# Kernel optimization log

Hardware: AMD Instinct MI355X
Metric: run time of the kernel (lower is better)

Reference implementation:

```python
import jax, jax.numpy as jnp
import numpy as np

N_NODES = 8192
N_EDGES = 262144
IN_DIM = 256
HID = 256
OUT_DIM = 64
PATH_DIM = 64
N_HEADS = 4


def setup_inputs() -> dict:
    key = jax.random.key(0)
    ks = jax.random.split(key, 16)
    s = 0.05
    x = jax.random.normal(ks[0], (N_NODES, IN_DIM), dtype=jnp.float32)
    edge_index = jax.random.randint(ks[1], (2, N_EDGES), 0, N_NODES, dtype=jnp.int32)
    return {
        "x": x,
        "edge_index": edge_index,
        # pathway encoder Linear(IN_DIM, PATH_DIM)
        "pe_w": jax.random.normal(ks[2], (IN_DIM, PATH_DIM), jnp.float32) * s,
        "pe_b": jax.random.normal(ks[3], (PATH_DIM,), jnp.float32) * s,
        # MultiheadAttention packed in-proj [3E, E] and out-proj [E, E]
        "in_proj_w": jax.random.normal(ks[4], (3 * PATH_DIM, PATH_DIM), jnp.float32) * s,
        "in_proj_b": jax.random.normal(ks[5], (3 * PATH_DIM,), jnp.float32) * s,
        "out_proj_w": jax.random.normal(ks[6], (PATH_DIM, PATH_DIM), jnp.float32) * s,
        "out_proj_b": jax.random.normal(ks[7], (PATH_DIM,), jnp.float32) * s,
        # GCN layer weights (in_dim, out_dim) + bias
        "w1": jax.random.normal(ks[8], (IN_DIM + PATH_DIM, HID), jnp.float32) * s,
        "b1": jax.random.normal(ks[9], (HID,), jnp.float32) * s,
        "w2": jax.random.normal(ks[10], (HID, HID), jnp.float32) * s,
        "b2": jax.random.normal(ks[11], (HID,), jnp.float32) * s,
        "w3": jax.random.normal(ks[12], (HID, OUT_DIM), jnp.float32) * s,
        "b3": jax.random.normal(ks[13], (OUT_DIM,), jnp.float32) * s,
    }


def mha_self(x, in_proj_w, in_proj_b, out_proj_w, out_proj_b):
    # unbatched nn.MultiheadAttention: x [N, E], Q=K=V=x
    N, E = x.shape
    dh = E // N_HEADS
    qkv = x @ in_proj_w.T + in_proj_b  # [N, 3E]
    q, k, v = jnp.split(qkv, 3, axis=-1)
    # [H, N, dh]
    q = q.reshape(N, N_HEADS, dh).transpose(1, 0, 2)
    k = k.reshape(N, N_HEADS, dh).transpose(1, 0, 2)
    v = v.reshape(N, N_HEADS, dh).transpose(1, 0, 2)
    scores = jnp.einsum('hnd,hmd->hnm', q, k) / jnp.sqrt(jnp.float32(dh))
    attn = jax.nn.softmax(scores, axis=-1)
    out = jnp.einsum('hnm,hmd->hnd', attn, v)  # [H, N, dh]
    out = out.transpose(1, 0, 2).reshape(N, E)
    return out @ out_proj_w.T + out_proj_b


def gcn_conv(h, edge_index, w, b, num_nodes):
    # PyG GCNConv: add self loops, symmetric normalization, linear, scatter-add, bias
    src = jnp.concatenate([edge_index[0], jnp.arange(num_nodes, dtype=edge_index.dtype)])
    dst = jnp.concatenate([edge_index[1], jnp.arange(num_nodes, dtype=edge_index.dtype)])
    deg = jax.ops.segment_sum(jnp.ones_like(dst, dtype=h.dtype), dst, num_segments=num_nodes)
    dinv = jnp.where(deg > 0, jax.lax.rsqrt(jnp.maximum(deg, 1e-12)), 0.0)
    hw = h @ w  # [N, out]
    norm = (dinv[src] * dinv[dst])[:, None]
    msg = hw[src] * norm
    out = jax.ops.segment_sum(msg, dst, num_segments=num_nodes)
    return out + b


def reference(x, edge_index, pe_w, pe_b, in_proj_w, in_proj_b, out_proj_w, out_proj_b,
              w1, b1, w2, b2, w3, b3):
    N = x.shape[0]
    pf = x @ pe_w + pe_b  # pathway encoder
    pa = mha_self(pf, in_proj_w, in_proj_b, out_proj_w, out_proj_b)
    h = jnp.concatenate([x, pa], axis=-1)  # [N, IN_DIM + PATH_DIM]
    h = jax.nn.relu(gcn_conv(h, edge_index, w1, b1, N))  # dropout is identity (eval)
    h = jax.nn.relu(gcn_conv(h, edge_index, w2, b2, N))
    h = gcn_conv(h, edge_index, w3, b3, N)
    return h
```

## Files before the change

kernel.cpp:

```cpp
#include <hip/hip_runtime.h>
#include <hip/hip_bf16.h>

#define N_NODES 8192
#define N_EDGES 262144
#define IN_DIM 256
#define HID 256
#define OUT_DIM 64
#define PATH_DIM 64
#define NHEADS 4
#define DH 16
#define KSPLIT 4

typedef __attribute__((ext_vector_type(8))) short bf16x8;
typedef __attribute__((ext_vector_type(4))) float f32x4;

__device__ __forceinline__ ushort f2bf(float f) {
  union { float f; unsigned int u; } c;
  c.f = f;
  unsigned int u = c.u;
  u += 0x7fffu + ((u >> 16) & 1u);
  return (ushort)(u >> 16);
}

__device__ __forceinline__ float fast_exp2(float x) {
  float r;
  asm("v_exp_f32 %0, %1" : "=v"(r) : "v"(x));
  return r;
}

__device__ __forceinline__ unsigned pack_bf16(float a, float b) {
  union { __hip_bfloat162 h; unsigned u; } c;
  c.h = __float22bfloat162_rn(make_float2(a, b));
  return c.u;
}


__global__ __launch_bounds__(256) void init_graph(int* deg, int* cursor) {
  int i = blockIdx.x * 256 + threadIdx.x;
  if (i < N_NODES) { deg[i] = 1; cursor[i] = 0; }
}

__global__ __launch_bounds__(256) void count_deg(const int* __restrict__ dst,
                                                 int* __restrict__ deg) {
  int e = blockIdx.x * 256 + threadIdx.x;
  if (e < N_EDGES) atomicAdd(&deg[dst[e]], 1);
}

__global__ __launch_bounds__(256) void scan_rows(const int* __restrict__ deg,
                                                 int* __restrict__ row_off,
                                                 float* __restrict__ dinv) {
  __shared__ int part[256];
  int t = threadIdx.x;
  int base = t * 32;
  int local[32];
  int s = 0;
  #pragma unroll
  for (int i = 0; i < 32; ++i) {
    int c = deg[base + i] - 1;
    local[i] = s;
    s += c;
  }
  part[t] = s;
  __syncthreads();
  for (int d = 1; d < 256; d <<= 1) {
    int v = (t >= d) ? part[t - d] : 0;
    __syncthreads();
    part[t] += v;
    __syncthreads();
  }
  int prev = (t == 0) ? 0 : part[t - 1];
  #pragma unroll
  for (int i = 0; i < 32; ++i) {
    row_off[base + i] = prev + local[i];
    dinv[base + i] = rsqrtf((float)deg[base + i]);
  }
}

__global__ __launch_bounds__(256) void fill_csr(const int* __restrict__ src,
                                                const int* __restrict__ dst,
                                                const int* __restrict__ row_off,
                                                int* __restrict__ cursor,
                                                int* __restrict__ csr) {
  int e = blockIdx.x * 256 + threadIdx.x;
  if (e < N_EDGES) {
    int d = dst[e];
    int p = atomicAdd(&cursor[d], 1);
    csr[row_off[d] + p] = src[e];
  }
}


__global__ __launch_bounds__(256) void transpose_w(const float* __restrict__ W,
                                                   float* __restrict__ Wt,
                                                   int R, int C) {
  int i = blockIdx.x * 256 + threadIdx.x;
  if (i < R * C) {
    int r = i / C, c = i % C;
    Wt[c * R + r] = W[i];
  }
}

__global__ __launch_bounds__(256) void convert_qkv(const float* __restrict__ qkv,
                                                   ushort* __restrict__ Qbf,
                                                   ushort* __restrict__ Kbf,
                                                   ushort* __restrict__ Vtb) {
  const int tg = blockIdx.x * 256 + threadIdx.x;
  const int h = tg >> 13;
  const int n = tg & 8191;
  const float SC = 0.36067376022224085f;
  const float* base = qkv + (size_t)n * 192 + h * 16;
  ushort* qd = Qbf + ((size_t)h * 8192 + n) * 32;
  ushort* kd = Kbf + ((size_t)h * 8192 + n) * 32;
  ushort4 zz = make_ushort4(0, 0, 0, 0);
  #pragma unroll
  for (int i = 0; i < 16; i += 4) {
    float4 q4 = *reinterpret_cast<const float4*>(base + i);
    float4 k4 = *reinterpret_cast<const float4*>(base + 64 + i);
    float4 v4 = *reinterpret_cast<const float4*>(base + 128 + i);
    *reinterpret_cast<ushort4*>(qd + i) =
        make_ushort4(f2bf(q4.x * SC), f2bf(q4.y * SC), f2bf(q4.z * SC), f2bf(q4.w * SC));
    *reinterpret_cast<ushort4*>(kd + i) =
        make_ushort4(f2bf(k4.x), f2bf(k4.y), f2bf(k4.z), f2bf(k4.w));
    *reinterpret_cast<ushort4*>(qd + 16 + i) = zz;
    *reinterpret_cast<ushort4*>(kd + 16 + i) = zz;
    Vtb[((size_t)h * 16 + i + 0) * 8192 + n] = f2bf(v4.x);
    Vtb[((size_t)h * 16 + i + 1) * 8192 + n] = f2bf(v4.y);
    Vtb[((size_t)h * 16 + i + 2) * 8192 + n] = f2bf(v4.z);
    Vtb[((size_t)h * 16 + i + 3) * 8192 + n] = f2bf(v4.w);
  }
}


template <bool RELU, bool BIAS>
__global__ __launch_bounds__(256) void gemm_tile(const float* __restrict__ A1, int K1,
                                                 const float* __restrict__ A2, int K2,
                                                 const float* __restrict__ B,
                                                 const float* __restrict__ bias,
                                                 float* __restrict__ C, int N) {
  __shared__ __align__(16) float As[16][64];
  __shared__ __align__(16) float Bs[16][68];
  const int K = K1 + K2;
  const int bm = blockIdx.y * 64;
  const int bn = blockIdx.x * 64;
  const int t = threadIdx.x;
  const int tx = t & 15, ty = t >> 4;
  const int am = t >> 2;
  const int ak = (t & 3) << 2;
  const int bk = t >> 4;
  const int bn4 = (t & 15) << 2;
  float acc[4][4] = {};
  for (int k0 = 0; k0 < K; k0 += 16) {
    int kk = k0 + ak;
    int row = bm + am;
    float4 av;
    if (kk < K1)
      av = *reinterpret_cast<const float4*>(A1 + (size_t)row * K1 + kk);
    else
      av = *reinterpret_cast<const float4*>(A2 + (size_t)row * K2 + (kk - K1));
    As[ak + 0][am] = av.x;
    As[ak + 1][am] = av.y;
    As[ak + 2][am] = av.z;
    As[ak + 3][am] = av.w;
    float4 bv = *reinterpret_cast<const float4*>(B + (size_t)(k0 + bk) * N + bn + bn4);
    *reinterpret_cast<float4*>(&Bs[bk][bn4]) = bv;
    __syncthreads();
    #pragma unroll
    for (int k = 0; k < 16; ++k) {
      float4 a = *reinterpret_cast<const float4*>(&As[k][ty << 2]);
      float4 b = *reinterpret_cast<const float4*>(&Bs[k][tx << 2]);
      acc[0][0] += a.x * b.x; acc[0][1] += a.x * b.y; acc[0][2] += a.x * b.z; acc[0][3] += a.x * b.w;
      acc[1][0] += a.y * b.x; acc[1][1] += a.y * b.y; acc[1][2] += a.y * b.z; acc[1][3] += a.y * b.w;
      acc[2][0] += a.z * b.x; acc[2][1] += a.z * b.y; acc[2][2] += a.z * b.z; acc[2][3] += a.z * b.w;
      acc[3][0] += a.w * b.x; acc[3][1] += a.w * b.y; acc[3][2] += a.w * b.z; acc[3][3] += a.w * b.w;
    }
    __syncthreads();
  }
  #pragma unroll
  for (int i = 0; i < 4; ++i) {
    int row = bm + (ty << 2) + i;
    float4 o = make_float4(acc[i][0], acc[i][1], acc[i][2], acc[i][3]);
    if (BIAS) {
      float4 bv = *reinterpret_cast<const float4*>(bias + bn + (tx << 2));
      o.x += bv.x; o.y += bv.y; o.z += bv.z; o.w += bv.w;
    }
    if (RELU) {
      o.x = fmaxf(o.x, 0.f); o.y = fmaxf(o.y, 0.f);
      o.z = fmaxf(o.z, 0.f); o.w = fmaxf(o.w, 0.f);
    }
    *reinterpret_cast<float4*>(C + (size_t)row * N + bn + (tx << 2)) = o;
  }
}


__global__ __launch_bounds__(256) void attn_mfma3(const ushort* __restrict__ Qbf,
                                                  const ushort* __restrict__ Kbf,
                                                  const ushort* __restrict__ Vtb,
                                                  float* __restrict__ Opart,
                                                  float* __restrict__ Wpart) {
  const int h  = blockIdx.y;
  const int qb = blockIdx.x;
  const int kz = blockIdx.z;
  const int t  = threadIdx.x;
  const int wv = t >> 6;
  const int l  = t & 63;
  const int lg = l >> 4;
  const int lc = l & 15;

  __shared__ __align__(16) ushort Ps[2][64][64];
  __shared__ __align__(16) ushort Vls[3][16][64];
  __shared__ float wred[4][64];

  bf16x8 qf[4];
  {
    const ushort* qbase = Qbf + ((size_t)h * 8192 + qb * 64) * 32;
    #pragma unroll
    for (int qt = 0; qt < 4; ++qt)
      qf[qt] = *reinterpret_cast<const bf16x8*>(qbase + (qt * 16 + lc) * 32 + lg * 8);
  }

  const ushort* kbase =
      Kbf + (size_t)h * 8192 * 32 + ((size_t)kz * 2048 + wv * 16 + lc) * 32 + lg * 8;

  const int vrow = t >> 4;
  const int vcol8 = t & 15;
  const ushort* vsrc = Vtb + ((size_t)h * 16 + vrow) * 8192 + kz * 2048 + vcol8 * 4;
  const int vdst = vrow * 128 + (((vcol8 >> 1) ^ (vrow & 7)) << 4) + (vcol8 & 1) * 8;

  const int pw_off = (((wv * 2 + (lg >> 1)) ^ (lc & 7)) << 4) + (lg & 1) * 8;
  int pr_off[2], vr_off[2];
  #pragma unroll
  for (int half = 0; half < 2; ++half) {
    int g = (half * 4 + lg) ^ (lc & 7);
    pr_off[half] = (wv * 16 + lc) * 128 + g * 16;
    vr_off[half] = lc * 128 + g * 16;
  }

  char* ps_base  = (char*)&Ps[0][0][0];
  char* vls_base = (char*)&Vls[0][0][0];

  *reinterpret_cast<ushort4*>(vls_base + vdst) =
      *reinterpret_cast<const ushort4*>(vsrc);

  f32x4 oacc = {0.f, 0.f, 0.f, 0.f};
  float wsumP[4] = {0.f, 0.f, 0.f, 0.f};

  __syncthreads();

  for (int c = 0; c < 2048 / 64; ++c) {
    const int mc = c * 64;
    ushort4 vpre;
    const bool dopre = (c + 1 < 2048 / 64);
    if (dopre) vpre = *reinterpret_cast<const ushort4*>(vsrc + mc + 64);

    bf16x8 kf = *reinterpret_cast<const bf16x8*>(kbase + (size_t)mc * 32);

    f32x4 s[4];
    #pragma unroll
    for (int qt = 0; qt < 4; ++qt) {
      f32x4 z = {0.f, 0.f, 0.f, 0.f};
      s[qt] = __builtin_amdgcn_mfma_f32_16x16x32_bf16(kf, qf[qt], z, 0, 0, 0);
    }

    char* psb = ps_base + (c & 1) * 8192;
    #pragma unroll
    for (int qt = 0; qt < 4; ++qt) {
      float e0 = fast_exp2(s[qt][0]);
      float e1 = fast_exp2(s[qt][1]);
      float e2 = fast_exp2(s[qt][2]);
      float e3 = fast_exp2(s[qt][3]);
      wsumP[qt] += (e0 + e1) + (e2 + e3);
      uint2 pk;
      pk.x = pack_bf16(e0, e1);
      pk.y = pack_bf16(e2, e3);
      *reinterpret_cast<uint2*>(psb + (qt * 16 + lc) * 128 + pw_off) = pk;
    }

    if (dopre)
      *reinterpret_cast<ushort4*>(vls_base + ((c + 1) % 3) * 2048 + vdst) = vpre;

    __syncthreads();

    char* vlb = vls_base + (c % 3) * 2048;
    #pragma unroll
    for (int half = 0; half < 2; ++half) {
      bf16x8 pf = *reinterpret_cast<const bf16x8*>(psb + pr_off[half]);
      bf16x8 vf = *reinterpret_cast<const bf16x8*>(vlb + vr_off[half]);
      oacc = __builtin_amdgcn_mfma_f32_16x16x32_bf16(pf, vf, oacc, 0, 0, 0);
    }
  }

  #pragma unroll
  for (int qt = 0; qt < 4; ++qt) {
    float v = wsumP[qt];
    v += __shfl_xor(v, 16);
    v += __shfl_xor(v, 32);
    wsumP[qt] = v;
  }
  if (lg == 0) {
    #pragma unroll
    for (int qt = 0; qt < 4; ++qt) wred[wv][qt * 16 + lc] = wsumP[qt];
  }
  __syncthreads();

  const size_t obase = ((size_t)(kz * NHEADS + h) * N_NODES + qb * 64);
  #pragma unroll
  for (int r = 0; r < 4; ++r) {
    const int qrow = wv * 16 + lg * 4 + r;
    Opart[(obase + qrow) * 16 + lc] = oacc[r];
  }
  if (t < 64) {
    float ws = wred[0][t] + wred[1][t] + wred[2][t] + wred[3][t];
    Wpart[obase + t] = ws;
  }
}

__global__ __launch_bounds__(256) void attn_combine(const float* __restrict__ Opart,
                                                    const float* __restrict__ Wpart,
                                                    float* __restrict__ attn_out) {
  int i = blockIdx.x * 256 + threadIdx.x;
  int dq = i & 3;
  int hn = i >> 2;
  int h = hn >> 13;
  int n = hn & 8191;
  float4 acc = make_float4(0.f, 0.f, 0.f, 0.f);
  float ws = 0.f;
  #pragma unroll
  for (int s = 0; s < KSPLIT; ++s) {
    const size_t row = ((size_t)(s * NHEADS + h) * N_NODES + n);
    float4 v = *reinterpret_cast<const float4*>(Opart + row * 16 + dq * 4);
    acc.x += v.x; acc.y += v.y; acc.z += v.z; acc.w += v.w;
    ws += Wpart[row];
  }
  float inv = 1.f / ws;
  float4 o = make_float4(acc.x * inv, acc.y * inv, acc.z * inv, acc.w * inv);
  *reinterpret_cast<float4*>(attn_out + (size_t)n * 64 + h * 16 + dq * 4) = o;
}


template <int C, bool RELU>
__global__ __launch_bounds__(256) void aggregate(const float* __restrict__ hw,
                                                 const int* __restrict__ csr,
                                                 const int* __restrict__ row_off,
                                                 const int* __restrict__ deg,
                                                 const float* __restrict__ dinv,
                                                 const float* __restrict__ bias,
                                                 float* __restrict__ out) {
  const int w = threadIdx.x >> 6, l = threadIdx.x & 63;
  const int r = blockIdx.x * 4 + w;
  const float dr = dinv[r];
  const int off = row_off[r];
  const int cnt = deg[r] - 1;

  if constexpr (C == 256) {
    const int c = l << 2;
    float4 a = *reinterpret_cast<const float4*>(hw + (size_t)r * C + c);
    float ax = dr * a.x, ay = dr * a.y, az = dr * a.z, aw = dr * a.w;
    for (int e = 0; e < cnt; ++e) {
      int s = csr[off + e];
      float ws = dinv[s];
      float4 hv = *reinterpret_cast<const float4*>(hw + (size_t)s * C + c);
      ax += ws * hv.x; ay += ws * hv.y; az += ws * hv.z; aw += ws * hv.w;
    }
    float4 bv = *reinterpret_cast<const float4*>(bias + c);
    float4 o;
    o.x = dr * ax + bv.x; o.y = dr * ay + bv.y;
    o.z = dr * az + bv.z; o.w = dr * aw + bv.w;
    if (RELU) {
      o.x = fmaxf(o.x, 0.f); o.y = fmaxf(o.y, 0.f);
      o.z = fmaxf(o.z, 0.f); o.w = fmaxf(o.w, 0.f);
    }
    *reinterpret_cast<float4*>(out + (size_t)r * C + c) = o;
  } else {
    float a = dr * hw[(size_t)r * C + l];
    for (int e = 0; e < cnt; ++e) {
      int s = csr[off + e];
      a += dinv[s] * hw[(size_t)s * C + l];
    }
    float o = dr * a + bias[l];
    if (RELU) o = fmaxf(o, 0.f);
    out[(size_t)r * C + l] = o;
  }
}


extern "C" void kernel_launch(void* const* d_in, const int* in_sizes, int n_in,
                              void* d_out, int out_size, void* d_ws, size_t ws_size,
                              hipStream_t stream) {
  const float* x          = (const float*)d_in[0];
  const int*   ei         = (const int*)d_in[1];
  const float* pe_w       = (const float*)d_in[2];
  const float* pe_b       = (const float*)d_in[3];
  const float* in_proj_w  = (const float*)d_in[4];
  const float* in_proj_b  = (const float*)d_in[5];
  const float* out_proj_w = (const float*)d_in[6];
  const float* out_proj_b = (const float*)d_in[7];
  const float* w1         = (const float*)d_in[8];
  const float* b1         = (const float*)d_in[9];
  const float* w2         = (const float*)d_in[10];
  const float* b2         = (const float*)d_in[11];
  const float* w3         = (const float*)d_in[12];
  const float* b3         = (const float*)d_in[13];

  const int* esrc = ei;
  const int* edst = ei + N_EDGES;

  char* ws = (char*)d_ws;
  size_t o = 0;
  auto take = [&](size_t n) {
    char* p = ws + o;
    o += (n + 255) & ~(size_t)255;
    return p;
  };
  float* pf       = (float*)take((size_t)N_NODES * PATH_DIM * 4);
  float* qkv      = (float*)take((size_t)N_NODES * 3 * PATH_DIM * 4);
  float* attn_out = (float*)take((size_t)N_NODES * PATH_DIM * 4);
  float* pa       = (float*)take((size_t)N_NODES * PATH_DIM * 4);
  float* hw       = (float*)take((size_t)N_NODES * HID * 4);
  float* h1       = (float*)take((size_t)N_NODES * HID * 4);
  float* h2       = (float*)take((size_t)N_NODES * HID * 4);
  float* Wt_in    = (float*)take((size_t)3 * PATH_DIM * PATH_DIM * 4);
  float* Wt_out   = (float*)take((size_t)PATH_DIM * PATH_DIM * 4);
  float* dinv     = (float*)take((size_t)N_NODES * 4);
  int*   deg      = (int*)take((size_t)N_NODES * 4);
  int*   cursor   = (int*)take((size_t)N_NODES * 4);
  int*   row_off  = (int*)take((size_t)N_NODES * 4);
  int*   csr      = (int*)take((size_t)N_EDGES * 4);

  ushort* Qbf = (ushort*)h1;
  ushort* Kbf = Qbf + (size_t)NHEADS * N_NODES * 32;
  ushort* Vtb = Kbf + (size_t)NHEADS * N_NODES * 32;
  float* Opart = h2;
  float* Wpart = pa;

  init_graph<<<N_NODES / 256, 256, 0, stream>>>(deg, cursor);
  count_deg<<<N_EDGES / 256, 256, 0, stream>>>(edst, deg);
  scan_rows<<<1, 256, 0, stream>>>(deg, row_off, dinv);
  fill_csr<<<N_EDGES / 256, 256, 0, stream>>>(esrc, edst, row_off, cursor, csr);

  transpose_w<<<(192 * 64 + 255) / 256, 256, 0, stream>>>(in_proj_w, Wt_in, 192, 64);
  transpose_w<<<(64 * 64 + 255) / 256, 256, 0, stream>>>(out_proj_w, Wt_out, 64, 64);

  gemm_tile<false, true><<<dim3(1, 128), 256, 0, stream>>>(x, IN_DIM, nullptr, 0, pe_w, pe_b, pf, PATH_DIM);
  gemm_tile<false, true><<<dim3(3, 128), 256, 0, stream>>>(pf, PATH_DIM, nullptr, 0, Wt_in, in_proj_b, qkv, 3 * PATH_DIM);

  convert_qkv<<<(N_NODES * NHEADS) / 256, 256, 0, stream>>>(qkv, Qbf, Kbf, Vtb);
  attn_mfma3<<<dim3(128, 4, KSPLIT), 256, 0, stream>>>(Qbf, Kbf, Vtb, Opart, Wpart);
  attn_combine<<<(NHEADS * N_NODES * 4) / 256, 256, 0, stream>>>(Opart, Wpart, attn_out);

  gemm_tile<false, true><<<dim3(1, 128), 256, 0, stream>>>(attn_out, PATH_DIM, nullptr, 0, Wt_out, out_proj_b, pa, PATH_DIM);

  gemm_tile<false, false><<<dim3(4, 128), 256, 0, stream>>>(x, IN_DIM, pa, PATH_DIM, w1, nullptr, hw, HID);
  aggregate<256, true><<<N_NODES / 4, 256, 0, stream>>>(hw, csr, row_off, deg, dinv, b1, h1);
  gemm_tile<false, false><<<dim3(4, 128), 256, 0, stream>>>(h1, HID, nullptr, 0, w2, nullptr, hw, HID);
  aggregate<256, true><<<N_NODES / 4, 256, 0, stream>>>(hw, csr, row_off, deg, dinv, b2, h2);
  gemm_tile<false, false><<<dim3(1, 128), 256, 0, stream>>>(h2, HID, nullptr, 0, w3, nullptr, hw, OUT_DIM);
  aggregate<64, false><<<N_NODES / 4, 256, 0, stream>>>(hw, csr, row_off, deg, dinv, b3, (float*)d_out);
}
```

Measured before the change: 304.0 us.

## Double attention key split, prefetch K fragments, and split GCN aggregation edges across two waves

The attention kernel now splits keys eight ways instead of four. It prefetches the next K fragment a chunk ahead, and it uses a single P buffer with two V buffers plus an extra barrier per chunk. The 256-wide GCN aggregation now gives each row two wavefronts that process alternating edges, and combines their partial sums through shared memory. This adds parallelism and memory-level concurrency to the latency-bound gather, at the cost of an extra barrier in the attention loop and a larger combine step. Workspace aliasing moves so the larger Opart fits in hw.

```diff
diff --git a/kernel.cpp b/kernel.cpp
--- a/kernel.cpp
+++ b/kernel.cpp
@@ -9,7 +9,9 @@
 #define PATH_DIM 64
 #define NHEADS 4
 #define DH 16
-#define KSPLIT 4
+#define KSPLIT 8
+#define SPLIT_KEYS (N_NODES / KSPLIT)
+#define NCHUNK (SPLIT_KEYS / 64)
 
 typedef __attribute__((ext_vector_type(8))) short bf16x8;
 typedef __attribute__((ext_vector_type(4))) float f32x4;
@@ -192,7 +194,7 @@
 }
 
 
-__global__ __launch_bounds__(256) void attn_mfma3(const ushort* __restrict__ Qbf,
+__global__ __launch_bounds__(256) void attn_mfma4(const ushort* __restrict__ Qbf,
                                                   const ushort* __restrict__ Kbf,
                                                   const ushort* __restrict__ Vtb,
                                                   float* __restrict__ Opart,
@@ -206,8 +208,8 @@
   const int lg = l >> 4;
   const int lc = l & 15;
 
-  __shared__ __align__(16) ushort Ps[2][64][64];
-  __shared__ __align__(16) ushort Vls[3][16][64];
+  __shared__ __align__(16) ushort Ps[64][64];
+  __shared__ __align__(16) ushort Vls[2][16][64];
   __shared__ float wred[4][64];
 
   bf16x8 qf[4];
@@ -219,11 +221,11 @@
   }
 
   const ushort* kbase =
-      Kbf + (size_t)h * 8192 * 32 + ((size_t)kz * 2048 + wv * 16 + lc) * 32 + lg * 8;
+      Kbf + (size_t)h * 8192 * 32 + ((size_t)kz * SPLIT_KEYS + wv * 16 + lc) * 32 + lg * 8;
 
   const int vrow = t >> 4;
   const int vcol8 = t & 15;
-  const ushort* vsrc = Vtb + ((size_t)h * 16 + vrow) * 8192 + kz * 2048 + vcol8 * 4;
+  const ushort* vsrc = Vtb + ((size_t)h * 16 + vrow) * 8192 + kz * SPLIT_KEYS + vcol8 * 4;
   const int vdst = vrow * 128 + (((vcol8 >> 1) ^ (vrow & 7)) << 4) + (vcol8 & 1) * 8;
 
   const int pw_off = (((wv * 2 + (lg >> 1)) ^ (lc & 7)) << 4) + (lg & 1) * 8;
@@ -235,24 +237,26 @@
     vr_off[half] = lc * 128 + g * 16;
   }
 
-  char* ps_base  = (char*)&Ps[0][0][0];
+  char* ps_base  = (char*)&Ps[0][0];
   char* vls_base = (char*)&Vls[0][0][0];
 
   *reinterpret_cast<ushort4*>(vls_base + vdst) =
       *reinterpret_cast<const ushort4*>(vsrc);
+  bf16x8 kf = *reinterpret_cast<const bf16x8*>(kbase);
 
   f32x4 oacc = {0.f, 0.f, 0.f, 0.f};
   float wsumP[4] = {0.f, 0.f, 0.f, 0.f};
 
   __syncthreads();
 
-  for (int c = 0; c < 2048 / 64; ++c) {
-    const int mc = c * 64;
+  for (int c = 0; c < NCHUNK; ++c) {
+    const bool more = (c + 1 < NCHUNK);
     ushort4 vpre;
-    const bool dopre = (c + 1 < 2048 / 64);
-    if (dopre) vpre = *reinterpret_cast<const ushort4*>(vsrc + mc + 64);
-
-    bf16x8 kf = *reinterpret_cast<const bf16x8*>(kbase + (size_t)mc * 32);
+    bf16x8 kf_n;
+    if (more) {
+      vpre = *reinterpret_cast<const ushort4*>(vsrc + (c + 1) * 64);
+      kf_n = *reinterpret_cast<const bf16x8*>(kbase + (size_t)(c + 1) * 64 * 32);
+    }
 
     f32x4 s[4];
     #pragma unroll
@@ -260,8 +264,8 @@
       f32x4 z = {0.f, 0.f, 0.f, 0.f};
       s[qt] = __builtin_amdgcn_mfma_f32_16x16x32_bf16(kf, qf[qt], z, 0, 0, 0);
     }
-
-    char* psb = ps_base + (c & 1) * 8192;
+    kf = kf_n;
+
     #pragma unroll
     for (int qt = 0; qt < 4; ++qt) {
       float e0 = fast_exp2(s[qt][0]);
@@ -272,21 +276,23 @@
       uint2 pk;
       pk.x = pack_bf16(e0, e1);
       pk.y = pack_bf16(e2, e3);
-      *reinterpret_cast<uint2*>(psb + (qt * 16 + lc) * 128 + pw_off) = pk;
-    }
-
-    if (dopre)
-      *reinterpret_cast<ushort4*>(vls_base + ((c + 1) % 3) * 2048 + vdst) = vpre;
-
-    __syncthreads();
-
-    char* vlb = vls_base + (c % 3) * 2048;
+      *reinterpret_cast<uint2*>(ps_base + (qt * 16 + lc) * 128 + pw_off) = pk;
+    }
+
+    if (more)
+      *reinterpret_cast<ushort4*>(vls_base + ((c + 1) & 1) * 2048 + vdst) = vpre;
+
+    __syncthreads();
+
+    char* vlb = vls_base + (c & 1) * 2048;
     #pragma unroll
     for (int half = 0; half < 2; ++half) {
-      bf16x8 pf = *reinterpret_cast<const bf16x8*>(psb + pr_off[half]);
+      bf16x8 pf = *reinterpret_cast<const bf16x8*>(ps_base + pr_off[half]);
       bf16x8 vf = *reinterpret_cast<const bf16x8*>(vlb + vr_off[half]);
       oacc = __builtin_amdgcn_mfma_f32_16x16x32_bf16(pf, vf, oacc, 0, 0, 0);
     }
+
+    __syncthreads();
   }
 
   #pragma unroll
@@ -337,49 +343,78 @@
 }
 
 
-template <int C, bool RELU>
-__global__ __launch_bounds__(256) void aggregate(const float* __restrict__ hw,
-                                                 const int* __restrict__ csr,
-                                                 const int* __restrict__ row_off,
-                                                 const int* __restrict__ deg,
-                                                 const float* __restrict__ dinv,
-                                                 const float* __restrict__ bias,
-                                                 float* __restrict__ out) {
+template <bool RELU>
+__global__ __launch_bounds__(256) void aggregate2(const float* __restrict__ hw,
+                                                  const int* __restrict__ csr,
+                                                  const int* __restrict__ row_off,
+                                                  const int* __restrict__ deg,
+                                                  const float* __restrict__ dinv,
+                                                  const float* __restrict__ bias,
+                                                  float* __restrict__ out) {
+  __shared__ __align__(16) float part[2][256];
+  const int t = threadIdx.x;
+  const int rw = t >> 7;
+  const int wh = (t >> 6) & 1;
+  const int l = t & 63;
+  const int r = blockIdx.x * 2 + rw;
+  const float dr = dinv[r];
+  const int off = row_off[r];
+  const int cnt = deg[r] - 1;
+  const int c = l << 2;
+
+  float ax, ay, az, aw;
+  if (wh == 0) {
+    float4 a = *reinterpret_cast<const float4*>(hw + (size_t)r * 256 + c);
+    ax = dr * a.x; ay = dr * a.y; az = dr * a.z; aw = dr * a.w;
+  } else {
+    ax = ay = az = aw = 0.f;
+  }
+  for (int e = wh; e < cnt; e += 2) {
+    int s = csr[off + e];
+    float wsc = dinv[s];
+    float4 hv = *reinterpret_cast<const float4*>(hw + (size_t)s * 256 + c);
+    ax += wsc * hv.x; ay += wsc * hv.y; az += wsc * hv.z; aw += wsc * hv.w;
+  }
+  if (wh == 1)
+    *reinterpret_cast<float4*>(&part[rw][c]) = make_float4(ax, ay, az, aw);
+  __syncthreads();
+  if (wh == 0) {
+    float4 p = *reinterpret_cast<const float4*>(&part[rw][c]);
+    float4 bv = *reinterpret_cast<const float4*>(bias + c);
+    float4 o;
+    o.x = dr * (ax + p.x) + bv.x;
+    o.y = dr * (ay + p.y) + bv.y;
+    o.z = dr * (az + p.z) + bv.z;
+    o.w = dr * (aw + p.w) + bv.w;
+    if (RELU) {
+      o.x = fmaxf(o.x, 0.f); o.y = fmaxf(o.y, 0.f);
+      o.z = fmaxf(o.z, 0.f); o.w = fmaxf(o.w, 0.f);
+    }
+    *reinterpret_cast<float4*>(out + (size_t)r * 256 + c) = o;
+  }
+}
+
+template <bool RELU>
+__global__ __launch_bounds__(256) void aggregate64(const float* __restrict__ hw,
+                                                   const int* __restrict__ csr,
+                                                   const int* __restrict__ row_off,
+                                                   const int* __restrict__ deg,
+                                                   const float* __restrict__ dinv,
+                                                   const float* __restrict__ bias,
+                                                   float* __restrict__ out) {
   const int w = threadIdx.x >> 6, l = threadIdx.x & 63;
   const int r = blockIdx.x * 4 + w;
   const float dr = dinv[r];
   const int off = row_off[r];
   const int cnt = deg[r] - 1;
-
-  if constexpr (C == 256) {
-    const int c = l << 2;
-    float4 a = *reinterpret_cast<const float4*>(hw + (size_t)r * C + c);
-    float ax = dr * a.x, ay = dr * a.y, az = dr * a.z, aw = dr * a.w;
-    for (int e = 0; e < cnt; ++e) {
-      int s = csr[off + e];
-      float ws = dinv[s];
-      float4 hv = *reinterpret_cast<const float4*>(hw + (size_t)s * C + c);
-      ax += ws * hv.x; ay += ws * hv.y; az += ws * hv.z; aw += ws * hv.w;
-    }
-    float4 bv = *reinterpret_cast<const float4*>(bias + c);
-    float4 o;
-    o.x = dr * ax + bv.x; o.y = dr * ay + bv.y;
-    o.z = dr * az + bv.z; o.w = dr * aw + bv.w;
-    if (RELU) {
-      o.x = fmaxf(o.x, 0.f); o.y = fmaxf(o.y, 0.f);
-      o.z = fmaxf(o.z, 0.f); o.w = fmaxf(o.w, 0.f);
-    }
-    *reinterpret_cast<float4*>(out + (size_t)r * C + c) = o;
-  } else {
-    float a = dr * hw[(size_t)r * C + l];
-    for (int e = 0; e < cnt; ++e) {
-      int s = csr[off + e];
-      a += dinv[s] * hw[(size_t)s * C + l];
-    }
-    float o = dr * a + bias[l];
-    if (RELU) o = fmaxf(o, 0.f);
-    out[(size_t)r * C + l] = o;
-  }
+  float a = dr * hw[(size_t)r * 64 + l];
+  for (int e = 0; e < cnt; ++e) {
+    int s = csr[off + e];
+    a += dinv[s] * hw[(size_t)s * 64 + l];
+  }
+  float o = dr * a + bias[l];
+  if (RELU) o = fmaxf(o, 0.f);
+  out[(size_t)r * 64 + l] = o;
 }
 
 
@@ -426,10 +461,10 @@
   int*   row_off  = (int*)take((size_t)N_NODES * 4);
   int*   csr      = (int*)take((size_t)N_EDGES * 4);
 
-  ushort* Qbf = (ushort*)h1;
+  ushort* Qbf = (ushort*)h2;
   ushort* Kbf = Qbf + (size_t)NHEADS * N_NODES * 32;
   ushort* Vtb = Kbf + (size_t)NHEADS * N_NODES * 32;
-  float* Opart = h2;
+  float* Opart = hw;
   float* Wpart = pa;
 
   init_graph<<<N_NODES / 256, 256, 0, stream>>>(deg, cursor);
@@ -444,15 +479,15 @@
   gemm_tile<false, true><<<dim3(3, 128), 256, 0, stream>>>(pf, PATH_DIM, nullptr, 0, Wt_in, in_proj_b, qkv, 3 * PATH_DIM);
 
   convert_qkv<<<(N_NODES * NHEADS) / 256, 256, 0, stream>>>(qkv, Qbf, Kbf, Vtb);
-  attn_mfma3<<<dim3(128, 4, KSPLIT), 256, 0, stream>>>(Qbf, Kbf, Vtb, Opart, Wpart);
+  attn_mfma4<<<dim3(128, 4, KSPLIT), 256, 0, stream>>>(Qbf, Kbf, Vtb, Opart, Wpart);
   attn_combine<<<(NHEADS * N_NODES * 4) / 256, 256, 0, stream>>>(Opart, Wpart, attn_out);
 
   gemm_tile<false, true><<<dim3(1, 128), 256, 0, stream>>>(attn_out, PATH_DIM, nullptr, 0, Wt_out, out_proj_b, pa, PATH_DIM);
 
   gemm_tile<false, false><<<dim3(4, 128), 256, 0, stream>>>(x, IN_DIM, pa, PATH_DIM, w1, nullptr, hw, HID);
-  aggregate<256, true><<<N_NODES / 4, 256, 0, stream>>>(hw, csr, row_off, deg, dinv, b1, h1);
+  aggregate2<true><<<N_NODES / 2, 256, 0, stream>>>(hw, csr, row_off, deg, dinv, b1, h1);
   gemm_tile<false, false><<<dim3(4, 128), 256, 0, stream>>>(h1, HID, nullptr, 0, w2, nullptr, hw, HID);
-  aggregate<256, true><<<N_NODES / 4, 256, 0, stream>>>(hw, csr, row_off, deg, dinv, b2, h2);
+  aggregate2<true><<<N_NODES / 2, 256, 0, stream>>>(hw, csr, row_off, deg, dinv, b2, h2);
   gemm_tile<false, false><<<dim3(1, 128), 256, 0, stream>>>(h2, HID, nullptr, 0, w3, nullptr, hw, OUT_DIM);
-  aggregate<64, false><<<N_NODES / 4, 256, 0, stream>>>(hw, csr, row_off, deg, dinv, b3, (float*)d_out);
-}
+  aggregate64<false><<<N_NODES / 4, 256, 0, stream>>>(hw, csr, row_off, deg, dinv, b3, (float*)d_out);
+}
```

New measurement: 296.7 us. 1.02x faster.
